# Performance work log

Measured on AMD Instinct MI355X. Metric: run time of the kernel, lower is better.

The kernel has to match this reference:

```python
import jax, jax.numpy as jnp
import numpy as np

B = 32768          # RL batch (many parallel env steps)
N = 12             # robot graph nodes (1 torso + 11 joint nodes)
D = 64             # node embedding dim
TORSO_DIM = 6
JOINT_DIM = 2
N_JOINTS = 11
OBS_DIM = TORSO_DIM + N_JOINTS * JOINT_DIM  # 28


def _build_adj_norm():
    # Ant-like tree: torso node 0, four legs of ~3 nodes each; edge_index was
    # built with self_loop=True and GCNConv uses add_self_loops=False, so we
    # symmetric-normalize (A + I).
    A = np.zeros((N, N), np.float32)
    edges = [(0, 1), (1, 2), (2, 3), (0, 4), (4, 5), (5, 6),
             (0, 7), (7, 8), (8, 9), (0, 10), (10, 11)]
    for i, j in edges:
        A[i, j] = 1.0
        A[j, i] = 1.0
    A += np.eye(N, dtype=np.float32)
    dinv = 1.0 / np.sqrt(A.sum(1))
    return jnp.asarray(A * dinv[:, None] * dinv[None, :])


def setup_inputs() -> dict:
    key = jax.random.key(0)
    ks = jax.random.split(key, 12)

    def w(k, shape):
        fan_in = shape[0]
        return jax.random.normal(k, shape, jnp.float32) / np.sqrt(fan_in)

    return {
        "observations": jax.random.normal(ks[0], (B, OBS_DIM), jnp.float32),
        "adj_norm": _build_adj_norm(),
        "w_in_torso": w(ks[1], (TORSO_DIM, D)), "b_in_torso": jnp.zeros((D,), jnp.float32),
        "w_in_joint": w(ks[2], (JOINT_DIM, D)), "b_in_joint": jnp.zeros((D,), jnp.float32),
        "w_gp1": w(ks[3], (D, D)), "b_gp1": jnp.zeros((D,), jnp.float32),
        "w_gp2": w(ks[4], (D, D)), "b_gp2": jnp.zeros((D,), jnp.float32),
        "w_gv1": w(ks[5], (D, D)), "b_gv1": jnp.zeros((D,), jnp.float32),
        "w_gv2": w(ks[6], (D, D)), "b_gv2": jnp.zeros((D,), jnp.float32),
        "w_pol1": w(ks[7], (D, D)), "b_pol1": jnp.zeros((D,), jnp.float32),
        "w_pol2": w(ks[8], (D, 1)), "b_pol2": jnp.zeros((1,), jnp.float32),
        "w_val1": w(ks[9], (N * D, D)), "b_val1": jnp.zeros((D,), jnp.float32),
        "w_val2": w(ks[10], (D, 1)), "b_val2": jnp.zeros((1,), jnp.float32),
    }


def reference(observations, adj_norm,
              w_in_torso, b_in_torso, w_in_joint, b_in_joint,
              w_gp1, b_gp1, w_gp2, b_gp2,
              w_gv1, b_gv1, w_gv2, b_gv2,
              w_pol1, b_pol1, w_pol2, b_pol2,
              w_val1, b_val1, w_val2, b_val2):
    b = observations.shape[0]
    # --- masked per-group node embedding (input model) ---
    obs_torso = observations[:, :TORSO_DIM]                              # [B,6]
    obs_joint = observations[:, TORSO_DIM:].reshape(b, N_JOINTS, JOINT_DIM)
    emb_t = jnp.tanh(obs_torso @ w_in_torso + b_in_torso)[:, None, :]    # [B,1,D]
    emb_j = jnp.tanh(jnp.einsum('bnf,fd->bnd', obs_joint, w_in_joint) + b_in_joint)
    x = jnp.concatenate([emb_t, emb_j], axis=1)                          # [B,N,D]

    # --- propagation model: GCNConv(x) = A_norm @ (x W) + b ---
    def gcn(h, W, bias):
        return jnp.einsum('nm,bmd->bnd', adj_norm, h @ W) + bias

    xp = jnp.tanh(gcn(x, w_gp1, b_gp1))
    xp = jnp.tanh(gcn(xp, w_gp2, b_gp2))                                 # policy GNN
    xv = jnp.tanh(gcn(x, w_gv1, b_gv1))
    xv = jnp.tanh(gcn(xv, w_gv2, b_gv2))                                 # value GNN

    # --- policy heads: one scalar per action (joint) node, shared group net ---
    act_emb = xp[:, 1:, :]                                               # [B,11,D]
    h = jnp.tanh(act_emb @ w_pol1 + b_pol1)
    latent_pi = (h @ w_pol2 + b_pol2)[..., 0]                            # [B,11]

    # --- value head: flatten all node embeddings ---
    flat = xv.reshape(b, N * D)                                          # [B,768]
    hv = jnp.tanh(flat @ w_val1 + b_val1)
    latent_vf = hv @ w_val2 + b_val2                                     # [B,1]
    return latent_pi, latent_vf
```

## Files before the change

kernel.cpp:

```cpp
#include <hip/hip_runtime.h>

#define NB 32768
#define NN 12
#define DD 64
#define OBSD 28
#define EPB 16
#define NSLOT 136

typedef __bf16 bf16x8 __attribute__((ext_vector_type(8)));
typedef __bf16 bf16x4 __attribute__((ext_vector_type(4)));
typedef __bf16 bf16x2 __attribute__((ext_vector_type(2)));
typedef float  f32x4  __attribute__((ext_vector_type(4)));
typedef float  f32x2  __attribute__((ext_vector_type(2)));

#define MFMA(a, b, c) __builtin_amdgcn_mfma_f32_16x16x32_bf16((a), (b), (c), 0, 0, 0)

__device__ __forceinline__ float tanh_fast(float x) {
    float e = __builtin_amdgcn_exp2f(x * 2.885390081777927f);
    float r = __builtin_amdgcn_rcpf(e + 1.f);
    return __builtin_fmaf(-2.f, r, 1.f);
}

static constexpr int AC_OFF[13] = {0,5,8,11,13,16,19,21,24,27,29,32,34};
static constexpr int AC_M[34] = {0,1,4,7,10, 0,1,2, 1,2,3, 2,3, 0,4,5, 4,5,6, 5,6, 0,7,8, 7,8,9, 8,9, 0,10,11, 10,11};
static constexpr int AC_N[34] = {0,0,0,0,0, 1,1,1, 2,2,2, 3,3, 4,4,4, 5,5,5, 6,6, 7,7,7, 8,8,8, 9,9, 10,10,10, 11,11};

__global__ __launch_bounds__(256) void prep_weights(
    const float* __restrict__ gp1, const float* __restrict__ gp2,
    const float* __restrict__ gv1, const float* __restrict__ gv2,
    const float* __restrict__ pol1, const float* __restrict__ val1,
    __bf16* __restrict__ wsb)
{
    int gid = blockIdx.x * blockDim.x + threadIdx.x;
    if (gid >= NSLOT * 64) return;
    int slot = gid >> 6, l = gid & 63;
    const float* W; int w, ks;
    if (slot < 32) {
        int m = slot >> 3;
        W = (m == 0) ? gp1 : (m == 1) ? gp2 : (m == 2) ? gv1 : gv2;
        w = (slot >> 1) & 3; ks = slot & 1;
    } else if (slot < 40) {
        W = pol1; w = (slot - 32) >> 1; ks = slot & 1;
    } else {
        int idx = slot - 40; W = val1; w = idx / 24; ks = idx % 24;
    }
    int dout = w * 16 + (l & 15);
    int k0 = ks * 32 + (l >> 4) * 8;
    bf16x8 v;
    #pragma unroll
    for (int i = 0; i < 8; ++i) v[i] = (__bf16)W[(size_t)(k0 + i) * 64 + dout];
    *(bf16x8*)(wsb + (size_t)gid * 8) = v;
}

__global__ __launch_bounds__(512, 6) void nervenet_mfma(
    const float* __restrict__ obs, const float* __restrict__ adjn,
    const float* __restrict__ w_in_t, const float* __restrict__ b_in_t,
    const float* __restrict__ w_in_j, const float* __restrict__ b_in_j,
    const float* __restrict__ b_gp1, const float* __restrict__ b_gp2,
    const float* __restrict__ b_gv1, const float* __restrict__ b_gv2,
    const float* __restrict__ b_pol1, const float* __restrict__ w_pol2, const float* __restrict__ b_pol2,
    const float* __restrict__ b_val1, const float* __restrict__ w_val2, const float* __restrict__ b_val2,
    const __bf16* __restrict__ wsb, float* __restrict__ out)
{
    __shared__ unsigned char X [EPB * NN * DD * 2];
    __shared__ unsigned char XP[EPB * NN * DD * 2];
    __shared__ float polp[4 * 11 * EPB];
    __shared__ float valp[4 * EPB];

    const int tid = threadIdx.x;
    const int l   = tid & 63;
    const int el  = l & 15;
    const int kg  = l >> 4;
    const int wv  = tid >> 6;
    const int w   = wv & 3;
    const bool isP = wv < 4;
    const int b0  = blockIdx.x * EPB;
    const int swz = (el & 7) << 4;

    auto ldws = [&](int slot) {
        return *(const bf16x8*)(wsb + ((size_t)slot * 64 + l) * 8);
    };

    const int sb1 = isP ? 0 : 16;
    const int sb2 = isP ? 8 : 24;
    const float* bias1 = isP ? b_gp1 : b_gv1;
    const float* bias2 = isP ? b_gp2 : b_gv2;
    bf16x8 wfA0 = ldws(sb1 + w * 2), wfA1 = ldws(sb1 + w * 2 + 1);
    bf16x8 wfB0 = ldws(sb2 + w * 2), wfB1 = ldws(sb2 + w * 2 + 1);
    f32x2 bA0 = *(const f32x2*)(bias1 + w * 16 + kg * 4);
    f32x2 bA1 = *(const f32x2*)(bias1 + w * 16 + kg * 4 + 2);
    f32x2 bB0 = *(const f32x2*)(bias2 + w * 16 + kg * 4);
    f32x2 bB1 = *(const f32x2*)(bias2 + w * 16 + kg * 4 + 2);

    float ac[34];
    #pragma unroll
    for (int i = 0; i < 34; ++i) ac[i] = adjn[AC_N[i] * 12 + AC_M[i]];

    {
        const int ee = tid & 15, fg = tid >> 4;
        const int eswz = (ee & 7) << 4;
        unsigned char* wp = X + (ee * NN) * 128 + ((fg * 4) ^ eswz);
        const float* os = obs + (size_t)(b0 + ee) * OBSD;
        f32x4 o0 = *(const f32x4*)(os);
        f32x4 o1 = *(const f32x4*)(os + 4);
        f32x4 o2 = *(const f32x4*)(os + 8);
        f32x4 o3 = *(const f32x4*)(os + 12);
        f32x4 o4 = *(const f32x4*)(os + 16);
        f32x4 o5 = *(const f32x4*)(os + 20);
        f32x4 o6 = *(const f32x4*)(os + 24);
        float tors[6] = {o0[0], o0[1], o0[2], o0[3], o1[0], o1[1]};
        float j0[11] = {o1[2], o2[0], o2[2], o3[0], o3[2], o4[0], o4[2], o5[0], o5[2], o6[0], o6[2]};
        float j1[11] = {o1[3], o2[1], o2[3], o3[1], o3[3], o4[1], o4[3], o5[1], o5[3], o6[1], o6[3]};

        f32x2 y = *(const f32x2*)(b_in_t + fg * 2);
        #pragma unroll
        for (int t = 0; t < 6; ++t) {
            f32x2 ob = {tors[t], tors[t]};
            y = __builtin_elementwise_fma(ob, *(const f32x2*)(w_in_t + t * DD + fg * 2), y);
        }
        bf16x2 t2;
        t2[0] = (__bf16)tanh_fast(y[0]); t2[1] = (__bf16)tanh_fast(y[1]);
        *(bf16x2*)(wp) = t2;

        f32x2 wj0 = *(const f32x2*)(w_in_j + fg * 2);
        f32x2 wj1 = *(const f32x2*)(w_in_j + DD + fg * 2);
        f32x2 bj  = *(const f32x2*)(b_in_j + fg * 2);
        #pragma unroll
        for (int n = 1; n < NN; ++n) {
            f32x2 a0 = {j0[n - 1], j0[n - 1]};
            f32x2 a1 = {j1[n - 1], j1[n - 1]};
            f32x2 yn = __builtin_elementwise_fma(a1, wj1,
                        __builtin_elementwise_fma(a0, wj0, bj));
            t2[0] = (__bf16)tanh_fast(yn[0]); t2[1] = (__bf16)tanh_fast(yn[1]);
            *(bf16x2*)(wp + n * 128) = t2;
        }
    }

    auto rdfrag = [&](const unsigned char* buf, int n, int ks) {
        return *(const bf16x8*)(buf + (el * NN + n) * 128 + ((ks * 64 + kg * 16) ^ swz));
    };

    f32x4 acc[NN];

    auto gcn_read = [&](const unsigned char* src, bf16x8 wf0, bf16x8 wf1) {
        #pragma unroll
        for (int n = 0; n < NN; ++n) {
            bf16x8 x0 = rdfrag(src, n, 0);
            bf16x8 x1 = rdfrag(src, n, 1);
            f32x4 a = {0.f, 0.f, 0.f, 0.f};
            a = MFMA(wf0, x0, a);
            a = MFMA(wf1, x1, a);
            acc[n] = a;
        }
    };
    auto gcn_write = [&](unsigned char* dst, f32x2 bv0, f32x2 bv1) {
        unsigned char* rowp = dst + (el * NN) * 128 + (((w * 16 + kg * 4) * 2) ^ swz);
        #pragma unroll
        for (int n = 0; n < NN; ++n) {
            f32x2 y0 = bv0, y1 = bv1;
            #pragma unroll
            for (int j = AC_OFF[n]; j < AC_OFF[n + 1]; ++j) {
                const float a = ac[j];
                f32x2 a2 = {a, a};
                const int m = AC_M[j];
                f32x2 lo = __builtin_shufflevector(acc[m], acc[m], 0, 1);
                f32x2 hi = __builtin_shufflevector(acc[m], acc[m], 2, 3);
                y0 = __builtin_elementwise_fma(a2, lo, y0);
                y1 = __builtin_elementwise_fma(a2, hi, y1);
            }
            bf16x4 o;
            o[0] = (__bf16)tanh_fast(y0[0]); o[1] = (__bf16)tanh_fast(y0[1]);
            o[2] = (__bf16)tanh_fast(y1[0]); o[3] = (__bf16)tanh_fast(y1[1]);
            *(bf16x4*)(rowp + n * 128) = o;
        }
    };

    unsigned char* MYBUF = isP ? XP : X;

    __syncthreads();
    gcn_read(X, wfA0, wfA1);
    __syncthreads();
    gcn_write(MYBUF, bA0, bA1);
    __syncthreads();
    gcn_read(MYBUF, wfB0, wfB1);
    __syncthreads();
    gcn_write(MYBUF, bB0, bB1);
    __syncthreads();

    {
        f32x4 bp  = *(const f32x4*)(b_pol1 + w * 16 + kg * 4);
        f32x4 wp2 = *(const f32x4*)(w_pol2 + w * 16 + kg * 4);
        bf16x8 pf0 = ldws(32 + w * 2 + 0);
        bf16x8 pf1 = ldws(32 + w * 2 + 1);
        auto pol_unit = [&](int nj) {
            bf16x8 x0 = rdfrag(XP, nj + 1, 0);
            bf16x8 x1 = rdfrag(XP, nj + 1, 1);
            f32x4 a = bp;
            a = MFMA(pf0, x0, a);
            a = MFMA(pf1, x1, a);
            float p = 0.f;
            #pragma unroll
            for (int r = 0; r < 4; ++r) p += tanh_fast(a[r]) * wp2[r];
            p += __shfl_xor(p, 16);
            p += __shfl_xor(p, 32);
            if (kg == 0) polp[w * 176 + nj * 16 + el] = p;
        };
        if (isP) {
            #pragma unroll
            for (int nj = 0; nj < 7; ++nj) pol_unit(nj);
        } else {
            #pragma unroll
            for (int nj = 7; nj < 11; ++nj) pol_unit(nj);
            f32x4 a0 = *(const f32x4*)(b_val1 + w * 16 + kg * 4);
            f32x4 a1 = {0.f, 0.f, 0.f, 0.f};
            #pragma unroll 4
            for (int ks = 0; ks < 24; ks += 2) {
                bf16x8 wf0 = ldws(40 + w * 24 + ks);
                bf16x8 wf1 = ldws(40 + w * 24 + ks + 1);
                int n = ks >> 1;
                bf16x8 xf0 = rdfrag(X, n, 0);
                bf16x8 xf1 = rdfrag(X, n, 1);
                a0 = MFMA(wf0, xf0, a0);
                a1 = MFMA(wf1, xf1, a1);
            }
            f32x4 wv2 = *(const f32x4*)(w_val2 + w * 16 + kg * 4);
            float p = 0.f;
            #pragma unroll
            for (int r = 0; r < 4; ++r) p += tanh_fast(a0[r] + a1[r]) * wv2[r];
            p += __shfl_xor(p, 16);
            p += __shfl_xor(p, 32);
            if (kg == 0) valp[w * 16 + el] = p;
        }
    }
    __syncthreads();

    if (tid < 176) {
        int e2 = tid / 11, nj = tid - e2 * 11;
        out[(size_t)b0 * 11 + tid] =
            polp[nj * 16 + e2] + polp[176 + nj * 16 + e2] +
            polp[352 + nj * 16 + e2] + polp[528 + nj * 16 + e2] + b_pol2[0];
    }
    if (tid >= 192 && tid < 192 + EPB) {
        int e2 = tid - 192;
        out[(size_t)NB * 11 + b0 + e2] =
            valp[e2] + valp[16 + e2] + valp[32 + e2] + valp[48 + e2] + b_val2[0];
    }
}

extern "C" void kernel_launch(void* const* d_in, const int* in_sizes, int n_in,
                              void* d_out, int out_size, void* d_ws, size_t ws_size,
                              hipStream_t stream) {
    (void)in_sizes; (void)n_in; (void)out_size; (void)ws_size;
    const float** p = (const float**)d_in;
    __bf16* wsb = (__bf16*)d_ws;
    hipLaunchKernelGGL(prep_weights, dim3(34), dim3(256), 0, stream,
        p[6], p[8], p[10], p[12], p[14], p[18], wsb);
    hipLaunchKernelGGL(nervenet_mfma, dim3(NB / EPB), dim3(512), 0, stream,
        p[0], p[1], p[2], p[3], p[4], p[5],
        p[7], p[9], p[11], p[13],
        p[15], p[16], p[17],
        p[19], p[20], p[21],
        wsb, (float*)d_out);
}
```

Baseline: 63.20 us.

## Use node-major LDS layout, fold tanh scale into weights, pack bf16 via cvt_pk

Changes the shared-memory activation layout from env-major to node-major, with row (n*EPB+el) instead of (el*NN+n). This alters LDS access strides and bank patterns for the fragment reads and writes. The tanh pre-scale constant is folded into the adjacency coefficients and biases, which removes one multiply per tanh in the GCN epilogue. Float-to-bf16 conversion now uses inline v_cvt_pk_bf16_f32 to pack pairs. The later head code (not shown) must also index the new layout; if it still uses the old indexing it would read the wrong rows.

Result: slower. 112.1 us (+77.3%).

```diff
diff --git a/kernel.cpp b/kernel.cpp
--- a/kernel.cpp
+++ b/kernel.cpp
@@ -15,8 +15,15 @@
 
 #define MFMA(a, b, c) __builtin_amdgcn_mfma_f32_16x16x32_bf16((a), (b), (c), 0, 0, 0)
 
+#define TSCALE 2.885390081777927f
+
 __device__ __forceinline__ float tanh_fast(float x) {
-    float e = __builtin_amdgcn_exp2f(x * 2.885390081777927f);
+    float e = __builtin_amdgcn_exp2f(x * TSCALE);
+    float r = __builtin_amdgcn_rcpf(e + 1.f);
+    return __builtin_fmaf(-2.f, r, 1.f);
+}
+__device__ __forceinline__ float tanh_pre(float y) {
+    float e = __builtin_amdgcn_exp2f(y);
     float r = __builtin_amdgcn_rcpf(e + 1.f);
     return __builtin_fmaf(-2.f, r, 1.f);
 }
@@ -62,8 +69,8 @@
     const float* __restrict__ b_val1, const float* __restrict__ w_val2, const float* __restrict__ b_val2,
     const __bf16* __restrict__ wsb, float* __restrict__ out)
 {
-    __shared__ unsigned char X [EPB * NN * DD * 2];
-    __shared__ unsigned char XP[EPB * NN * DD * 2];
+    __shared__ unsigned char X [NN * EPB * DD * 2];
+    __shared__ unsigned char XP[NN * EPB * DD * 2];
     __shared__ float polp[4 * 11 * EPB];
     __shared__ float valp[4 * EPB];
 
@@ -87,19 +94,20 @@
     const float* bias2 = isP ? b_gp2 : b_gv2;
     bf16x8 wfA0 = ldws(sb1 + w * 2), wfA1 = ldws(sb1 + w * 2 + 1);
     bf16x8 wfB0 = ldws(sb2 + w * 2), wfB1 = ldws(sb2 + w * 2 + 1);
-    f32x2 bA0 = *(const f32x2*)(bias1 + w * 16 + kg * 4);
-    f32x2 bA1 = *(const f32x2*)(bias1 + w * 16 + kg * 4 + 2);
-    f32x2 bB0 = *(const f32x2*)(bias2 + w * 16 + kg * 4);
-    f32x2 bB1 = *(const f32x2*)(bias2 + w * 16 + kg * 4 + 2);
+    const f32x2 ts2 = {TSCALE, TSCALE};
+    f32x2 bA0 = *(const f32x2*)(bias1 + w * 16 + kg * 4)     * ts2;
+    f32x2 bA1 = *(const f32x2*)(bias1 + w * 16 + kg * 4 + 2) * ts2;
+    f32x2 bB0 = *(const f32x2*)(bias2 + w * 16 + kg * 4)     * ts2;
+    f32x2 bB1 = *(const f32x2*)(bias2 + w * 16 + kg * 4 + 2) * ts2;
 
     float ac[34];
     #pragma unroll
-    for (int i = 0; i < 34; ++i) ac[i] = adjn[AC_N[i] * 12 + AC_M[i]];
+    for (int i = 0; i < 34; ++i) ac[i] = adjn[AC_N[i] * 12 + AC_M[i]] * TSCALE;
 
     {
         const int ee = tid & 15, fg = tid >> 4;
         const int eswz = (ee & 7) << 4;
-        unsigned char* wp = X + (ee * NN) * 128 + ((fg * 4) ^ eswz);
+        unsigned char* wp = X + ee * 128 + ((fg * 4) ^ eswz);
         const float* os = obs + (size_t)(b0 + ee) * OBSD;
         f32x4 o0 = *(const f32x4*)(os);
         f32x4 o1 = *(const f32x4*)(os + 4);
@@ -132,12 +140,12 @@
             f32x2 yn = __builtin_elementwise_fma(a1, wj1,
                         __builtin_elementwise_fma(a0, wj0, bj));
             t2[0] = (__bf16)tanh_fast(yn[0]); t2[1] = (__bf16)tanh_fast(yn[1]);
-            *(bf16x2*)(wp + n * 128) = t2;
+            *(bf16x2*)(wp + n * (EPB * 128)) = t2;
         }
     }
 
     auto rdfrag = [&](const unsigned char* buf, int n, int ks) {
-        return *(const bf16x8*)(buf + (el * NN + n) * 128 + ((ks * 64 + kg * 16) ^ swz));
+        return *(const bf16x8*)(buf + (n * EPB + el) * 128 + ((ks * 64 + kg * 16) ^ swz));
     };
 
     f32x4 acc[NN];
@@ -154,7 +162,7 @@
         }
     };
     auto gcn_write = [&](unsigned char* dst, f32x2 bv0, f32x2 bv1) {
-        unsigned char* rowp = dst + (el * NN) * 128 + (((w * 16 + kg * 4) * 2) ^ swz);
+        unsigned char* colp = dst + el * 128 + (((w * 16 + kg * 4) * 2) ^ swz);
         #pragma unroll
         for (int n = 0; n < NN; ++n) {
             f32x2 y0 = bv0, y1 = bv1;
@@ -168,10 +176,12 @@
                 y0 = __builtin_elementwise_fma(a2, lo, y0);
                 y1 = __builtin_elementwise_fma(a2, hi, y1);
             }
-            bf16x4 o;
-            o[0] = (__bf16)tanh_fast(y0[0]); o[1] = (__bf16)tanh_fast(y0[1]);
-            o[2] = (__bf16)tanh_fast(y1[0]); o[3] = (__bf16)tanh_fast(y1[1]);
-            *(bf16x4*)(rowp + n * 128) = o;
+            float t0 = tanh_pre(y0[0]), t1 = tanh_pre(y0[1]);
+            float t2 = tanh_pre(y1[0]), t3 = tanh_pre(y1[1]);
+            uint2 pk;
+            asm("v_cvt_pk_bf16_f32 %0, %1, %2" : "=v"(pk.x) : "v"(t0), "v"(t1));
+            asm("v_cvt_pk_bf16_f32 %0, %1, %2" : "=v"(pk.y) : "v"(t2), "v"(t3));
+            *(uint2*)(colp + n * (EPB * 128)) = pk;
         }
     };
 
```
